# Performance work log

Hardware: AMD Instinct MI355X
Metric: run time of the kernel (lower is better)

Reference implementation:

```python
import jax, jax.numpy as jnp
import numpy as np

N_NODES = 50000
N_EDGES = 800000
IN_CH = 64
HID = 128
LAST_HID = 256


def setup_inputs() -> dict:
    key = jax.random.key(0)
    ks = jax.random.split(key, 12)
    x = jax.random.normal(ks[0], (N_NODES, IN_CH), dtype=jnp.float32)
    edge_index = jax.random.randint(ks[1], (2, N_EDGES), 0, N_NODES, dtype=jnp.int64)
    s = lambda fan_in: 1.0 / np.sqrt(fan_in)
    return {
        "x": x,
        "edge_index": edge_index,
        # SAGEConv1: lin_l (aggregated neighbors, with bias), lin_r (root, no bias)
        "W1l": jax.random.normal(ks[2], (HID, IN_CH), dtype=jnp.float32) * s(IN_CH),
        "b1l": jnp.zeros((HID,), dtype=jnp.float32),
        "W1r": jax.random.normal(ks[3], (HID, IN_CH), dtype=jnp.float32) * s(IN_CH),
        # SAGEConv2 -> 1 channel
        "W2l": jax.random.normal(ks[4], (1, HID), dtype=jnp.float32) * s(HID),
        "b2l": jnp.zeros((1,), dtype=jnp.float32),
        "W2r": jax.random.normal(ks[5], (1, HID), dtype=jnp.float32) * s(HID),
        # fc1 (LazyLinear bound to N_NODES input features) and fc2
        "fc1_W": jax.random.normal(ks[6], (LAST_HID, N_NODES), dtype=jnp.float32) * s(N_NODES),
        "fc1_b": jnp.zeros((LAST_HID,), dtype=jnp.float32),
        "fc2_W": jax.random.normal(ks[7], (1, LAST_HID), dtype=jnp.float32) * s(LAST_HID),
        "fc2_b": jnp.zeros((1,), dtype=jnp.float32),
    }


def _sage_conv(h, src, dst, Wl, bl, Wr, n_nodes):
    # PyG SAGEConv (mean aggr): out = lin_l(mean_{j in N(i)} x_j) + lin_r(x_i)
    msgs = h[src]  # [E, F] gather of source node features
    summed = jax.ops.segment_sum(msgs, dst, num_segments=n_nodes)  # [N, F]
    deg = jax.ops.segment_sum(jnp.ones((src.shape[0],), h.dtype), dst, num_segments=n_nodes)
    agg = summed / jnp.maximum(deg, 1.0)[:, None]
    return agg @ Wl.T + bl + h @ Wr.T


def reference(x, edge_index, W1l, b1l, W1r, W2l, b2l, W2r, fc1_W, fc1_b, fc2_W, fc2_b):
    n = x.shape[0]
    src, dst = edge_index[0], edge_index[1]
    h = jax.nn.relu(_sage_conv(x, src, dst, W1l, b1l, W1r, n))   # [N, HID]
    h = jax.nn.relu(_sage_conv(h, src, dst, W2l, b2l, W2r, n))   # [N, 1]
    v = h[:, 0]                                                   # [N]
    z = fc1_W @ v + fc1_b                                         # [LAST_HID]
    pred = fc2_W @ z + fc2_b                                      # [1]
    return pred[0]  # scalar (torch.squeeze)
```

## Files before the change

kernel.cpp:

```cpp
#include <hip/hip_runtime.h>

#define N_NODESC 50000
#define N_EDGESC 800000
#define MAXDEG 64

typedef short bf16x8 __attribute__((ext_vector_type(8)));
typedef short short4v __attribute__((ext_vector_type(4)));
typedef float f32x4  __attribute__((ext_vector_type(4)));

__device__ inline unsigned short f2bf(float f) {
    unsigned u = __float_as_uint(f);
    unsigned r = u + 0x7FFFu + ((u >> 16) & 1u);
    return (unsigned short)(r >> 16);
}
__device__ inline float bf2f(unsigned short h) {
    return __uint_as_float(((unsigned)h) << 16);
}

__global__ void kW0_init_pack(const float* __restrict__ x,
                              const float* __restrict__ W1l, const float* __restrict__ W1r,
                              short* __restrict__ pkhi, short* __restrict__ pklo,
                              unsigned short* __restrict__ xb,
                              int* __restrict__ deg, float* __restrict__ z) {
    int i = blockIdx.x * 256 + threadIdx.x;
    if (i < N_NODESC) deg[i] = 0;
    if (i < 256) z[i] = 0.0f;

    int base = i * 16;
    if (base < N_NODESC * 64) {
        const float* src = x + base;
        bf16x8 h0, h1;
        #pragma unroll
        for (int j = 0; j < 2; j++) {
            float4 a = *(const float4*)(src + j * 8);
            float4 b = *(const float4*)(src + j * 8 + 4);
            bf16x8& hh = j ? h1 : h0;
            hh[0] = (short)f2bf(a.x); hh[1] = (short)f2bf(a.y);
            hh[2] = (short)f2bf(a.z); hh[3] = (short)f2bf(a.w);
            hh[4] = (short)f2bf(b.x); hh[5] = (short)f2bf(b.y);
            hh[6] = (short)f2bf(b.z); hh[7] = (short)f2bf(b.w);
        }
        *(bf16x8*)(xb + base) = h0;
        *(bf16x8*)(xb + base + 8) = h1;
    }

    if (blockIdx.x < 4) {
        int ks = blockIdx.x;
        int t  = threadIdx.x;
        int o  = t & 127;
        int h  = t >> 7;
        const float* src = (ks < 2) ? (W1r + o * 64 + ks * 32)
                                    : (W1l + o * 64 + (ks - 2) * 32);
        #pragma unroll
        for (int qi = 0; qi < 2; qi++) {
            int q = 2 * h + qi;
            float4 a = *(const float4*)(src + q * 8);
            float4 b = *(const float4*)(src + q * 8 + 4);
            float v[8] = {a.x, a.y, a.z, a.w, b.x, b.y, b.z, b.w};
            bf16x8 hv, lv;
            #pragma unroll
            for (int j = 0; j < 8; j++) {
                unsigned short hh = f2bf(v[j]);
                hv[j] = (short)hh;
                lv[j] = (short)f2bf(v[j] - bf2f(hh));
            }
            int idx = ((ks * 4 + q) * 128 + o) * 8;
            *(bf16x8*)&pkhi[idx] = hv;
            *(bf16x8*)&pklo[idx] = lv;
        }
    }
}

#define K1_BLOCKS 2048
#define K1_EPB (N_EDGESC / (K1_BLOCKS / 8))
__global__ void k1_bucket(const int* __restrict__ ei, int* __restrict__ deg,
                          unsigned short* __restrict__ bucket) {
    int g   = blockIdx.x & 7;
    int idx = blockIdx.x >> 3;
    int lo = g * (N_NODESC / 8), hi = lo + (N_NODESC / 8);
    int e0 = idx * K1_EPB;
    for (int i = threadIdx.x; i < K1_EPB; i += 256) {
        int e = e0 + i;
        int dst = ei[N_EDGESC + e];
        if (dst >= lo && dst < hi) {
            int src = ei[e];
            int slot = atomicAdd(&deg[dst], 1);
            if (slot < MAXDEG) bucket[dst * MAXDEG + slot] = (unsigned short)src;
        }
    }
}

#define K3S 144
#define K3BLK 32

__launch_bounds__(512, 4)
__global__ void k3_fused(const float* __restrict__ x, const unsigned short* __restrict__ xb,
                         const int* __restrict__ deg, const unsigned short* __restrict__ bucket,
                         const short* __restrict__ pkhi, const short* __restrict__ pklo,
                         const float* __restrict__ b1l,
                         const float* __restrict__ W2l, const float* __restrict__ W2r,
                         float* __restrict__ s_out, float* __restrict__ t_out) {
    __shared__ __align__(16) short sAhi[K3BLK * K3S];
    __shared__ __align__(16) short sAlo[K3BLK * K3S];
    __shared__ float sSp[8][K3BLK], sTp[8][K3BLK];

    int tid = threadIdx.x;
    int lane = tid & 63;
    int wave = tid >> 6;
    int col = lane & 15;
    int quad = lane >> 4;
    int node0 = blockIdx.x * K3BLK;

    float4 sv;
    {
        int n = tid >> 4, kc = tid & 15;
        int node = node0 + n;
        if (node < N_NODESC) {
            sv = *(const float4*)(x + node * 64 + kc * 4);
        } else {
            sv = make_float4(0.f, 0.f, 0.f, 0.f);
        }
    }
    {
        int n = tid >> 4, kc = tid & 15;
        float v[4] = {sv.x, sv.y, sv.z, sv.w};
        short4v hv, lv;
        #pragma unroll
        for (int j = 0; j < 4; j++) {
            unsigned short h = f2bf(v[j]);
            hv[j] = (short)h;
            lv[j] = (short)f2bf(v[j] - bf2f(h));
        }
        *(short4v*)&sAhi[n * K3S + kc * 4] = hv;
        *(short4v*)&sAlo[n * K3S + kc * 4] = lv;
    }

    {
        int base = node0 + wave * 4;
        int dd[4], cc[4];
        int bb[4];
        #pragma unroll
        for (int c = 0; c < 4; c++) {
            int nd = base + c;
            dd[c] = 0; bb[c] = 0;
            if (nd < N_NODESC) {
                dd[c] = deg[nd];
                bb[c] = (int)bucket[nd * MAXDEG + lane];
            }
        }
        int kmax = 0;
        #pragma unroll
        for (int c = 0; c < 4; c++) { cc[c] = min(dd[c], MAXDEG); kmax = max(kmax, cc[c]); }

        float4 av[4];
        #pragma unroll
        for (int c = 0; c < 4; c++) av[c] = make_float4(0.f, 0.f, 0.f, 0.f);

        for (int k = 0; k < kmax; k += 8) {
            int i0 = k + quad, i1 = k + 4 + quad;
            #pragma unroll
            for (int c = 0; c < 4; c++) {
                int s0 = __shfl(bb[c], i0);
                int s1 = __shfl(bb[c], i1);
                if (i0 < cc[c]) {
                    short4v hv_ = *(const short4v*)(xb + s0 * 64 + col * 4);
                    av[c].x += bf2f((unsigned short)hv_[0]);
                    av[c].y += bf2f((unsigned short)hv_[1]);
                    av[c].z += bf2f((unsigned short)hv_[2]);
                    av[c].w += bf2f((unsigned short)hv_[3]);
                }
                if (i1 < cc[c]) {
                    short4v hv_ = *(const short4v*)(xb + s1 * 64 + col * 4);
                    av[c].x += bf2f((unsigned short)hv_[0]);
                    av[c].y += bf2f((unsigned short)hv_[1]);
                    av[c].z += bf2f((unsigned short)hv_[2]);
                    av[c].w += bf2f((unsigned short)hv_[3]);
                }
            }
        }
        #pragma unroll
        for (int c = 0; c < 4; c++) {
            #pragma unroll
            for (int m = 16; m <= 32; m <<= 1) {
                av[c].x += __shfl_xor(av[c].x, m);
                av[c].y += __shfl_xor(av[c].y, m);
                av[c].z += __shfl_xor(av[c].z, m);
                av[c].w += __shfl_xor(av[c].w, m);
            }
        }
        if (quad == 0) {
            #pragma unroll
            for (int c = 0; c < 4; c++) {
                int nloc = wave * 4 + c;
                float inv = 1.0f / (float)max(dd[c], 1);
                float vv[4] = {av[c].x * inv, av[c].y * inv, av[c].z * inv, av[c].w * inv};
                short4v hv, lv;
                #pragma unroll
                for (int j = 0; j < 4; j++) {
                    unsigned short h = f2bf(vv[j]);
                    hv[j] = (short)h;
                    lv[j] = (short)f2bf(vv[j] - bf2f(h));
                }
                *(short4v*)&sAhi[nloc * K3S + 64 + col * 4] = hv;
                *(short4v*)&sAlo[nloc * K3S + 64 + col * 4] = lv;
            }
        }
    }

    int o = wave * 16 + col;
    bf16x8 bhi[4], blo[4];
    float bias_r = b1l[o], w2l_r = W2l[o], w2r_r = W2r[o];
    #pragma unroll
    for (int ks = 0; ks < 4; ks++) {
        int idx = ((ks * 4 + quad) * 128 + o) * 8;
        bhi[ks] = *(const bf16x8*)&pkhi[idx];
        blo[ks] = *(const bf16x8*)&pklo[idx];
    }
    __syncthreads();

    f32x4 acc[2];
    acc[0] = (f32x4)0.f;
    acc[1] = (f32x4)0.f;

    #pragma unroll
    for (int ks = 0; ks < 4; ks++) {
        #pragma unroll
        for (int nt = 0; nt < 2; nt++) {
            int off = (nt * 16 + col) * K3S + ks * 32 + quad * 8;
            bf16x8 ah = *(const bf16x8*)&sAhi[off];
            bf16x8 al = *(const bf16x8*)&sAlo[off];
            acc[nt] = __builtin_amdgcn_mfma_f32_16x16x32_bf16(ah, bhi[ks], acc[nt], 0, 0, 0);
            acc[nt] = __builtin_amdgcn_mfma_f32_16x16x32_bf16(al, bhi[ks], acc[nt], 0, 0, 0);
            acc[nt] = __builtin_amdgcn_mfma_f32_16x16x32_bf16(ah, blo[ks], acc[nt], 0, 0, 0);
        }
    }

    #pragma unroll
    for (int nt = 0; nt < 2; nt++) {
        float sp[4], tp[4];
        #pragma unroll
        for (int reg = 0; reg < 4; reg++) {
            float h = fmaxf(acc[nt][reg] + bias_r, 0.f);
            sp[reg] = h * w2l_r;
            tp[reg] = h * w2r_r;
        }
        #pragma unroll
        for (int reg = 0; reg < 4; reg++) {
            #pragma unroll
            for (int m = 1; m <= 8; m <<= 1) {
                sp[reg] += __shfl_xor(sp[reg], m);
                tp[reg] += __shfl_xor(tp[reg], m);
            }
        }
        if (col == 0) {
            int nn = nt * 16 + quad * 4;
            #pragma unroll
            for (int reg = 0; reg < 4; reg++) {
                sSp[wave][nn + reg] = sp[reg];
                sTp[wave][nn + reg] = tp[reg];
            }
        }
    }
    __syncthreads();
    if (tid < K3BLK) {
        int node = node0 + tid;
        if (node < N_NODESC) {
            float ssum = 0.f, tsum = 0.f;
            #pragma unroll
            for (int w = 0; w < 8; w++) { ssum += sSp[w][tid]; tsum += sTp[w][tid]; }
            s_out[node] = ssum;
            t_out[node] = tsum;
        }
    }
}

__global__ void k4_layer2(const float* __restrict__ s, const float* __restrict__ t,
                          const int* __restrict__ deg, const unsigned short* __restrict__ bucket,
                          const float* __restrict__ b2l, float* __restrict__ v) {
    int tid = threadIdx.x;
    int lane = tid & 15;
    int node = blockIdx.x * 16 + (tid >> 4);
    int d = deg[node];
    int c = min(d, MAXDEG);
    float sum = 0.f;
    for (int k = lane; k < c; k += 16) sum += s[bucket[node * MAXDEG + k]];
    sum += __shfl_xor(sum, 1);
    sum += __shfl_xor(sum, 2);
    sum += __shfl_xor(sum, 4);
    sum += __shfl_xor(sum, 8);
    if (lane == 0) {
        float h = sum / (float)max(d, 1) + b2l[0] + t[node];
        v[node] = fmaxf(h, 0.f);
    }
}

__global__ void k5_fc1(const float* __restrict__ fc1W, const float* __restrict__ v,
                       float* __restrict__ z) {
    int row = blockIdx.x >> 2;
    int part = blockIdx.x & 3;
    const float4* W4 = (const float4*)(fc1W + row * 50000 + part * 12500);
    const float4* v4 = (const float4*)(v + part * 12500);
    float sum = 0.f;
    for (int i = threadIdx.x; i < 3125; i += 256) {
        float4 w = W4[i], a = v4[i];
        sum += w.x * a.x + w.y * a.y + w.z * a.z + w.w * a.w;
    }
    #pragma unroll
    for (int m = 1; m < 64; m <<= 1) sum += __shfl_xor(sum, m);
    __shared__ float red[4];
    if ((threadIdx.x & 63) == 0) red[threadIdx.x >> 6] = sum;
    __syncthreads();
    if (threadIdx.x == 0) atomicAdd(&z[row], red[0] + red[1] + red[2] + red[3]);
}

__global__ void k6_head(const float* __restrict__ z, const float* __restrict__ fc1b,
                        const float* __restrict__ fc2W, const float* __restrict__ fc2b,
                        float* __restrict__ out) {
    int t = threadIdx.x;
    float val = (z[t] + fc1b[t]) * fc2W[t];
    #pragma unroll
    for (int m = 1; m < 64; m <<= 1) val += __shfl_xor(val, m);
    __shared__ float red[4];
    if ((t & 63) == 0) red[t >> 6] = val;
    __syncthreads();
    if (t == 0) out[0] = red[0] + red[1] + red[2] + red[3] + fc2b[0];
}

extern "C" void kernel_launch(void* const* d_in, const int* in_sizes, int n_in,
                              void* d_out, int out_size, void* d_ws, size_t ws_size,
                              hipStream_t stream) {
    const float* x    = (const float*)d_in[0];
    const int*   ei   = (const int*)d_in[1];
    const float* W1l  = (const float*)d_in[2];
    const float* b1l  = (const float*)d_in[3];
    const float* W1r  = (const float*)d_in[4];
    const float* W2l  = (const float*)d_in[5];
    const float* b2l  = (const float*)d_in[6];
    const float* W2r  = (const float*)d_in[7];
    const float* fc1W = (const float*)d_in[8];
    const float* fc1b = (const float*)d_in[9];
    const float* fc2W = (const float*)d_in[10];
    const float* fc2b = (const float*)d_in[11];
    float* out = (float*)d_out;

    char* ws = (char*)d_ws;
    int*            deg    = (int*)           (ws + 0);
    float*          z      = (float*)         (ws + 200192);
    unsigned short* bucket = (unsigned short*)(ws + 201216);
    unsigned short* xb     = (unsigned short*)(ws + 6601216);
    float*          s      = (float*)         (ws + 13001216);
    float*          t      = (float*)         (ws + 13201216);
    float*          v      = (float*)         (ws + 13401216);
    short*          pkhi   = (short*)         (ws + 13601280);
    short*          pklo   = (short*)         (ws + 13634048);

    kW0_init_pack<<<782,  256, 0, stream>>>(x, W1l, W1r, pkhi, pklo, xb, deg, z);
    k1_bucket    <<<K1_BLOCKS, 256, 0, stream>>>(ei, deg, bucket);
    k3_fused     <<<1563, 512, 0, stream>>>(x, xb, deg, bucket, pkhi, pklo, b1l, W2l, W2r, s, t);
    k4_layer2    <<<3125, 256, 0, stream>>>(s, t, deg, bucket, b2l, v);
    k5_fc1       <<<1024, 256, 0, stream>>>(fc1W, v, z);
    k6_head      <<<1,    256, 0, stream>>>(z, fc1b, fc2W, fc2b, out);
}
```

Baseline: 205.0 us.

## Stage neighbor buckets in LDS and gather one channel per lane

```diff
diff --git a/kernel.cpp b/kernel.cpp
--- a/kernel.cpp
+++ b/kernel.cpp
@@ -6,6 +6,7 @@
 
 typedef short bf16x8 __attribute__((ext_vector_type(8)));
 typedef short short4v __attribute__((ext_vector_type(4)));
+typedef unsigned short ushort4v __attribute__((ext_vector_type(4)));
 typedef float f32x4  __attribute__((ext_vector_type(4)));
 
 __device__ inline unsigned short f2bf(float f) {
@@ -102,6 +103,8 @@
                          float* __restrict__ s_out, float* __restrict__ t_out) {
     __shared__ __align__(16) short sAhi[K3BLK * K3S];
     __shared__ __align__(16) short sAlo[K3BLK * K3S];
+    __shared__ __align__(16) unsigned short sBkt[K3BLK * 64];
+    __shared__ int sDeg[K3BLK];
     __shared__ float sSp[8][K3BLK], sTp[8][K3BLK];
 
     int tid = threadIdx.x;
@@ -121,6 +124,24 @@
             sv = make_float4(0.f, 0.f, 0.f, 0.f);
         }
     }
+
+    {
+        int off = tid * 4;
+        int glim = (N_NODESC - node0) * 64;
+        if (off + 4 <= glim) {
+            *(ushort4v*)&sBkt[off] = *(const ushort4v*)&bucket[node0 * 64 + off];
+        } else {
+            #pragma unroll
+            for (int k = 0; k < 4; k++)
+                sBkt[off + k] = (off + k < glim) ? bucket[node0 * 64 + off + k]
+                                                 : (unsigned short)0;
+        }
+        if (tid < K3BLK) {
+            int node = node0 + tid;
+            sDeg[tid] = (node < N_NODESC) ? deg[node] : 0;
+        }
+    }
+
     {
         int n = tid >> 4, kc = tid & 15;
         float v[4] = {sv.x, sv.y, sv.z, sv.w};
@@ -134,77 +155,38 @@
         *(short4v*)&sAhi[n * K3S + kc * 4] = hv;
         *(short4v*)&sAlo[n * K3S + kc * 4] = lv;
     }
-
-    {
-        int base = node0 + wave * 4;
-        int dd[4], cc[4];
-        int bb[4];
-        #pragma unroll
-        for (int c = 0; c < 4; c++) {
-            int nd = base + c;
-            dd[c] = 0; bb[c] = 0;
-            if (nd < N_NODESC) {
-                dd[c] = deg[nd];
-                bb[c] = (int)bucket[nd * MAXDEG + lane];
-            }
-        }
-        int kmax = 0;
-        #pragma unroll
-        for (int c = 0; c < 4; c++) { cc[c] = min(dd[c], MAXDEG); kmax = max(kmax, cc[c]); }
-
-        float4 av[4];
-        #pragma unroll
-        for (int c = 0; c < 4; c++) av[c] = make_float4(0.f, 0.f, 0.f, 0.f);
-
-        for (int k = 0; k < kmax; k += 8) {
-            int i0 = k + quad, i1 = k + 4 + quad;
-            #pragma unroll
-            for (int c = 0; c < 4; c++) {
-                int s0 = __shfl(bb[c], i0);
-                int s1 = __shfl(bb[c], i1);
-                if (i0 < cc[c]) {
-                    short4v hv_ = *(const short4v*)(xb + s0 * 64 + col * 4);
-                    av[c].x += bf2f((unsigned short)hv_[0]);
-                    av[c].y += bf2f((unsigned short)hv_[1]);
-                    av[c].z += bf2f((unsigned short)hv_[2]);
-                    av[c].w += bf2f((unsigned short)hv_[3]);
-                }
-                if (i1 < cc[c]) {
-                    short4v hv_ = *(const short4v*)(xb + s1 * 64 + col * 4);
-                    av[c].x += bf2f((unsigned short)hv_[0]);
-                    av[c].y += bf2f((unsigned short)hv_[1]);
-                    av[c].z += bf2f((unsigned short)hv_[2]);
-                    av[c].w += bf2f((unsigned short)hv_[3]);
-                }
-            }
-        }
-        #pragma unroll
-        for (int c = 0; c < 4; c++) {
-            #pragma unroll
-            for (int m = 16; m <= 32; m <<= 1) {
-                av[c].x += __shfl_xor(av[c].x, m);
-                av[c].y += __shfl_xor(av[c].y, m);
-                av[c].z += __shfl_xor(av[c].z, m);
-                av[c].w += __shfl_xor(av[c].w, m);
-            }
-        }
-        if (quad == 0) {
-            #pragma unroll
-            for (int c = 0; c < 4; c++) {
-                int nloc = wave * 4 + c;
-                float inv = 1.0f / (float)max(dd[c], 1);
-                float vv[4] = {av[c].x * inv, av[c].y * inv, av[c].z * inv, av[c].w * inv};
-                short4v hv, lv;
-                #pragma unroll
-                for (int j = 0; j < 4; j++) {
-                    unsigned short h = f2bf(vv[j]);
-                    hv[j] = (short)h;
-                    lv[j] = (short)f2bf(vv[j] - bf2f(h));
-                }
-                *(short4v*)&sAhi[nloc * K3S + 64 + col * 4] = hv;
-                *(short4v*)&sAlo[nloc * K3S + 64 + col * 4] = lv;
-            }
-        }
+    __syncthreads();
+
+    #pragma unroll
+    for (int c4 = 0; c4 < 4; c4++) {
+        int nloc = wave * 4 + c4;
+        int d = sDeg[nloc];
+        int c = min(d, MAXDEG);
+        float a0 = 0.f, a1 = 0.f, a2 = 0.f, a3 = 0.f;
+        float a4 = 0.f, a5 = 0.f, a6 = 0.f, a7 = 0.f;
+        int j = 0;
+        for (; j + 8 <= c; j += 8) {
+            ushort4v q0 = *(const ushort4v*)&sBkt[nloc * 64 + j];
+            ushort4v q1 = *(const ushort4v*)&sBkt[nloc * 64 + j + 4];
+            a0 += bf2f(xb[(int)q0[0] * 64 + lane]);
+            a1 += bf2f(xb[(int)q0[1] * 64 + lane]);
+            a2 += bf2f(xb[(int)q0[2] * 64 + lane]);
+            a3 += bf2f(xb[(int)q0[3] * 64 + lane]);
+            a4 += bf2f(xb[(int)q1[0] * 64 + lane]);
+            a5 += bf2f(xb[(int)q1[1] * 64 + lane]);
+            a6 += bf2f(xb[(int)q1[2] * 64 + lane]);
+            a7 += bf2f(xb[(int)q1[3] * 64 + lane]);
+        }
+        for (; j < c; j++) {
+            a0 += bf2f(xb[(int)sBkt[nloc * 64 + j] * 64 + lane]);
+        }
+        float av = ((a0 + a1) + (a2 + a3)) + ((a4 + a5) + (a6 + a7));
+        float inv = 1.0f / (float)max(d, 1);
+        float m = av * inv;
+        unsigned short h = f2bf(m);
+        unsigned short l = f2bf(m - bf2f(h));
+        sAhi[nloc * K3S + 64 + lane] = (short)h;
+        sAlo[nloc * K3S + 64 + lane] = (short)l;
     }
 
     int o = wave * 16 + col;
```

After: 203.8 us. About the same (-0.6%).
